# Kernel tuning notes

Measured on AMD Instinct MI355X. Metric: run time of the kernel, lower is better.

## Reference

```python
import jax, jax.numpy as jnp
import numpy as np

DIM = 1024
HEADS = 16
HEAD_DIM = DIM // HEADS
MLP_HIDDEN = int(DIM * 0.7)  # 716
EPS = 1e-5


def _ln(x, g, b):
    m = jnp.mean(x, axis=-1, keepdims=True)
    v = jnp.mean(jnp.square(x - m), axis=-1, keepdims=True)
    return (x - m) * jax.lax.rsqrt(v + EPS) * g + b


def setup_inputs() -> dict:
    key = jax.random.key(0)
    ks = jax.random.split(key, 8)
    B, N = 4, 1024
    x = jax.random.normal(ks[0], (B, N, DIM), dtype=jnp.float32)
    s = 0.02
    return {
        "x": x,
        "norm_g": jnp.ones((DIM,), jnp.float32),
        "norm_b": jnp.zeros((DIM,), jnp.float32),
        "W1": jax.random.normal(ks[1], (DIM, 3 * DIM + MLP_HIDDEN), jnp.float32) * s,
        "b1": jnp.zeros((3 * DIM + MLP_HIDDEN,), jnp.float32),
        "qn_g": jnp.ones((HEAD_DIM,), jnp.float32),
        "qn_b": jnp.zeros((HEAD_DIM,), jnp.float32),
        "kn_g": jnp.ones((HEAD_DIM,), jnp.float32),
        "kn_b": jnp.zeros((HEAD_DIM,), jnp.float32),
        "projW": jax.random.normal(ks[2], (DIM, DIM), jnp.float32) * s,
        "projb": jnp.zeros((DIM,), jnp.float32),
        "mlpW": jax.random.normal(ks[3], (MLP_HIDDEN, DIM), jnp.float32) * s,  # mlp_bias=False
        "W2": jax.random.normal(ks[4], (2 * DIM, DIM), jnp.float32) * s,
        "b2": jnp.zeros((DIM,), jnp.float32),
        "ls_g": jnp.full((DIM,), 1e-5, jnp.float32),
    }


def reference(x, norm_g, norm_b, W1, b1, qn_g, qn_b, kn_g, kn_b,
              projW, projb, mlpW, W2, b2, ls_g):
    B, N, C = x.shape
    norm_x = _ln(x, norm_g, norm_b)
    f1 = norm_x @ W1 + b1  # (B, N, 3*dim + mlp_hidden)
    qkv, mlp_hidden = f1[..., :3 * DIM], f1[..., 3 * DIM:]
    # (B, N, 3, H, hd) -> (3, B, H, N, hd)
    qkv = qkv.reshape(B, N, 3, HEADS, HEAD_DIM).transpose(2, 0, 3, 1, 4)
    q, k, v = qkv[0], qkv[1], qkv[2]
    q = _ln(q, qn_g, qn_b)
    k = _ln(k, kn_g, kn_b)
    attn = jnp.einsum('bhnd,bhmd->bhnm', q, k) * (HEAD_DIM ** -0.5)
    attn = jax.nn.softmax(attn, axis=-1)
    xo = jnp.einsum('bhnm,bhmd->bhnd', attn, v)
    xo = xo.transpose(0, 2, 1, 3).reshape(B, N, DIM)
    attn_out = xo @ projW + projb
    mlp_out = jax.nn.gelu(mlp_hidden, approximate=False) @ mlpW  # no bias
    combined = jnp.concatenate([attn_out, mlp_out], axis=-1)
    out = x + (combined @ W2 + b2) * ls_g
    return out
```

## Files before the change

### kernel.cpp

```cpp
#include <hip/hip_runtime.h>
#include <cstdint>
#include <cstddef>

typedef unsigned short u16;
typedef unsigned char u8;
typedef __attribute__((ext_vector_type(8))) u16 u16x8;
typedef __attribute__((ext_vector_type(8))) __bf16 bf16x8;
typedef __attribute__((ext_vector_type(4))) float f32x4;
typedef __attribute__((ext_vector_type(16))) float f32x16;
typedef __attribute__((ext_vector_type(4))) int i32x4;
typedef __attribute__((ext_vector_type(8))) int i32x8;

__device__ __forceinline__ u16 f2bf(float f) {
  unsigned u = __builtin_bit_cast(unsigned, f);
  return (u16)((u + 0x7FFFu + ((u >> 16) & 1u)) >> 16);
}
__device__ __forceinline__ float bf2f(u16 h) {
  return __builtin_bit_cast(float, (unsigned)h << 16);
}
__device__ __forceinline__ u8 f2fp8(float f) {
  return (u8)(__builtin_amdgcn_cvt_pk_fp8_f32(f, 0.f, 0, false) & 0xFF);
}
__device__ __forceinline__ f32x4 mfma16(u16x8 a, u16x8 b, f32x4 c) {
  return __builtin_amdgcn_mfma_f32_16x16x32_bf16(
      __builtin_bit_cast(bf16x8, a), __builtin_bit_cast(bf16x8, b), c, 0, 0, 0);
}
__device__ __forceinline__ void load_lds16(const void* g, void* l) {
  __builtin_amdgcn_global_load_lds(
      (const __attribute__((address_space(1))) void*)g,
      (__attribute__((address_space(3))) void*)l, 16, 0, 0);
}

__global__ __launch_bounds__(256) void k_trcvt_all(
    const float* __restrict__ W1, const float* __restrict__ projW,
    const float* __restrict__ mlpW, const float* __restrict__ W2,
    u8* __restrict__ W1t, u8* __restrict__ pWt, u8* __restrict__ mWt,
    u8* __restrict__ W2t) {
  __shared__ float t[32][33];
  const int L = blockIdx.x;
  const float* src;
  u8* dst;
  int R, C, dR, dC, bx, by;
  if (L < 3840) {
    src = W1; dst = W1t; R = 1024; C = 3788; dR = 1024; dC = 3840;
    bx = L % 120; by = L / 120;
  } else if (L < 4864) {
    int tq = L - 3840;
    src = projW; dst = pWt; R = 1024; C = 1024; dR = 1024; dC = 1024;
    bx = tq & 31; by = tq >> 5;
  } else if (L < 5632) {
    int tq = L - 4864;
    src = mlpW; dst = mWt; R = 716; C = 1024; dR = 768; dC = 1024;
    bx = tq & 31; by = tq >> 5;
  } else {
    int tq = L - 5632;
    src = W2; dst = W2t; R = 2048; C = 1024; dR = 2048; dC = 1024;
    bx = tq & 31; by = tq >> 5;
  }
  const int n0 = bx * 32, k0 = by * 32;
  const int tx = threadIdx.x & 31, ty = threadIdx.x >> 5;
#pragma unroll
  for (int j = 0; j < 4; ++j) {
    int kk = k0 + ty + 8 * j, nn = n0 + tx;
    float v = (kk < R && nn < C) ? src[(size_t)kk * C + nn] : 0.f;
    t[ty + 8 * j][tx] = v;
  }
  __syncthreads();
#pragma unroll
  for (int j = 0; j < 4; ++j) {
    int nn = n0 + ty + 8 * j, kk = k0 + tx;
    if (nn < dC && kk < dR) dst[(size_t)nn * dR + kk] = f2fp8(t[tx][ty + 8 * j]);
  }
}

__global__ __launch_bounds__(256) void k_trvt(const u16* __restrict__ f1,
                                              u16* __restrict__ vtb) {
  __shared__ u16 t[32][33];
  const int z = blockIdx.z;
  const int b = z >> 4, h = z & 15;
  const int d0 = blockIdx.x * 32, n0 = blockIdx.y * 32;
  const int tx = threadIdx.x & 31, ty = threadIdx.x >> 5;
#pragma unroll
  for (int j = 0; j < 4; ++j)
    t[ty + 8 * j][tx] =
        f1[(size_t)(b * 1024 + n0 + ty + 8 * j) * 3840 + 2048 + h * 64 + d0 + tx];
  __syncthreads();
#pragma unroll
  for (int j = 0; j < 4; ++j)
    vtb[(size_t)z * 65536 + (size_t)(d0 + ty + 8 * j) * 1024 + n0 + tx] =
        t[tx][ty + 8 * j];
}

__global__ __launch_bounds__(256) void k_lnx(const float* __restrict__ x,
                                             const float* __restrict__ g,
                                             const float* __restrict__ b,
                                             u8* __restrict__ out) {
  const int row = blockIdx.x, tid = threadIdx.x;
  float4 v = ((const float4*)(x + (size_t)row * 1024))[tid];
  float s = v.x + v.y + v.z + v.w;
  float ss = v.x * v.x + v.y * v.y + v.z * v.z + v.w * v.w;
#pragma unroll
  for (int off = 1; off < 64; off <<= 1) {
    s += __shfl_xor(s, off);
    ss += __shfl_xor(ss, off);
  }
  __shared__ float red[8];
  const int wid = tid >> 6, lane = tid & 63;
  if (lane == 0) { red[wid] = s; red[4 + wid] = ss; }
  __syncthreads();
  s = red[0] + red[1] + red[2] + red[3];
  ss = red[4] + red[5] + red[6] + red[7];
  const float mean = s * (1.f / 1024.f);
  const float var = ss * (1.f / 1024.f) - mean * mean;
  const float rstd = rsqrtf(var + 1e-5f);
  float4 gv = ((const float4*)g)[tid];
  float4 bv = ((const float4*)b)[tid];
  float y0 = (v.x - mean) * rstd * gv.x + bv.x;
  float y1 = (v.y - mean) * rstd * gv.y + bv.y;
  float y2 = (v.z - mean) * rstd * gv.z + bv.z;
  float y3 = (v.w - mean) * rstd * gv.w + bv.w;
  int pk = __builtin_amdgcn_cvt_pk_fp8_f32(y0, y1, 0, false);
  pk = __builtin_amdgcn_cvt_pk_fp8_f32(y2, y3, pk, true);
  ((int*)(out + (size_t)row * 1024))[tid] = pk;
}

__device__ __forceinline__ void gemm_fp8_core(const u8* __restrict__ A,
                                              const u8* __restrict__ B, int K,
                                              u8* Alds, u8* Blds,
                                              f32x16 (&acc)[2][2], int tid) {
  const int lane = tid & 63, wave = tid >> 6;
  const int h = lane >> 5, r32 = lane & 31;
  const int wrow = (wave >> 1) * 64, wcol = (wave & 1) * 64;
  const int srow0 = tid >> 2, spos = tid & 3;
  const int nk = K >> 6;
  for (int kt = 0; kt < nk; ++kt) {
#pragma unroll
    for (int p = 0; p < 2; ++p) {
      const int row = p * 64 + srow0;
      const int c = spos ^ ((row >> 1) & 3);
      const size_t go = (size_t)row * K + kt * 64 + c * 16;
      load_lds16(A + go, Alds + (p * 256 + tid) * 16);
      load_lds16(B + go, Blds + (p * 256 + tid) * 16);
    }
    __syncthreads();
    i32x8 af[2], bf[2];
#pragma unroll
    for (int t = 0; t < 2; ++t) {
      {
        const int row = wrow + t * 32 + r32;
        const int sw = (row >> 1) & 3;
        i32x4 lo = *(const i32x4*)(Alds + row * 64 + ((2 * h) ^ sw) * 16);
        i32x4 hi = *(const i32x4*)(Alds + row * 64 + ((2 * h + 1) ^ sw) * 16);
        i32x8 a;
        a[0] = lo[0]; a[1] = lo[1]; a[2] = lo[2]; a[3] = lo[3];
        a[4] = hi[0]; a[5] = hi[1]; a[6] = hi[2]; a[7] = hi[3];
        af[t] = a;
      }
      {
        const int row = wcol + t * 32 + r32;
        const int sw = (row >> 1) & 3;
        i32x4 lo = *(const i32x4*)(Blds + row * 64 + ((2 * h) ^ sw) * 16);
        i32x4 hi = *(const i32x4*)(Blds + row * 64 + ((2 * h + 1) ^ sw) * 16);
        i32x8 b8;
        b8[0] = lo[0]; b8[1] = lo[1]; b8[2] = lo[2]; b8[3] = lo[3];
        b8[4] = hi[0]; b8[5] = hi[1]; b8[6] = hi[2]; b8[7] = hi[3];
        bf[t] = b8;
      }
    }
#pragma unroll
    for (int i = 0; i < 2; ++i)
#pragma unroll
      for (int j = 0; j < 2; ++j)
        acc[i][j] = __builtin_amdgcn_mfma_scale_f32_32x32x64_f8f6f4(
            af[i], bf[j], acc[i][j], 0, 0, 0, 0x7F7F7F7F, 0, 0x7F7F7F7F);
    __syncthreads();
  }
}

__global__ __launch_bounds__(256) void k_gemm1(const u8* __restrict__ nx8,
                                               const u8* __restrict__ W1t,
                                               u16* __restrict__ f1,
                                               const float* __restrict__ b1) {
  __shared__ __align__(16) u8 Alds[128 * 64];
  __shared__ __align__(16) u8 Blds[128 * 64];
  const int tid = threadIdx.x, bm = blockIdx.y, bn = blockIdx.x;
  f32x16 acc[2][2];
#pragma unroll
  for (int i = 0; i < 2; ++i)
#pragma unroll
    for (int j = 0; j < 2; ++j)
#pragma unroll
      for (int r = 0; r < 16; ++r) acc[i][j][r] = 0.f;
  gemm_fp8_core(nx8 + (size_t)bm * 128 * 1024, W1t + (size_t)bn * 128 * 1024, 1024,
                Alds, Blds, acc, tid);
  const int lane = tid & 63, wave = tid >> 6;
  const int h = lane >> 5, r32 = lane & 31;
  const int wrow = (wave >> 1) * 64, wcol = (wave & 1) * 64;
#pragma unroll
  for (int i = 0; i < 2; ++i)
#pragma unroll
    for (int j = 0; j < 2; ++j) {
      const int col = bn * 128 + wcol + j * 32 + r32;
      const float bs = (col < 3788) ? b1[col] : 0.f;
#pragma unroll
      for (int r = 0; r < 16; ++r) {
        const int row = bm * 128 + wrow + i * 32 + 4 * h + (r & 3) + 8 * (r >> 2);
        f1[(size_t)row * 3840 + col] = f2bf(acc[i][j][r] + bs);
      }
    }
}

__global__ __launch_bounds__(256) void k_gemm_pm(
    const u8* __restrict__ xo, const u8* __restrict__ pWt,
    const u8* __restrict__ gel, const u8* __restrict__ mWt,
    u8* __restrict__ comb, const float* __restrict__ projb) {
  __shared__ __align__(16) u8 Alds[128 * 64];
  __shared__ __align__(16) u8 Blds[128 * 64];
  const int tid = threadIdx.x, bm = blockIdx.y, bnq = blockIdx.x;
  const u8* A;
  const u8* B;
  int K, colbase;
  const float* bias;
  if (bnq < 8) {
    A = xo + (size_t)bm * 128 * 1024;
    B = pWt + (size_t)bnq * 128 * 1024;
    K = 1024; colbase = bnq * 128; bias = projb;
  } else {
    A = gel + (size_t)bm * 128 * 768;
    B = mWt + (size_t)(bnq - 8) * 128 * 768;
    K = 768; colbase = 1024 + (bnq - 8) * 128; bias = nullptr;
  }
  f32x16 acc[2][2];
#pragma unroll
  for (int i = 0; i < 2; ++i)
#pragma unroll
    for (int j = 0; j < 2; ++j)
#pragma unroll
      for (int r = 0; r < 16; ++r) acc[i][j][r] = 0.f;
  gemm_fp8_core(A, B, K, Alds, Blds, acc, tid);
  const int lane = tid & 63, wave = tid >> 6;
  const int h = lane >> 5, r32 = lane & 31;
  const int wrow = (wave >> 1) * 64, wcol = (wave & 1) * 64;
#pragma unroll
  for (int i = 0; i < 2; ++i)
#pragma unroll
    for (int j = 0; j < 2; ++j) {
      const int col = colbase + wcol + j * 32 + r32;
      const float bs = (bias != nullptr) ? bias[col - colbase + colbase -
                                               (bias == projb ? 0 : 0)] : 0.f;
      const float bsv = (bias != nullptr) ? bias[wcol + j * 32 + r32 + 0 +
                                                 (colbase - colbase)] : 0.f;
      (void)bs;
#pragma unroll
      for (int r = 0; r < 16; ++r) {
        const int row = bm * 128 + wrow + i * 32 + 4 * h + (r & 3) + 8 * (r >> 2);
        float v = acc[i][j][r] + ((bias != nullptr) ? bias[col] : 0.f);
        (void)bsv;
        comb[(size_t)row * 2048 + col] = f2fp8(v);
      }
    }
}

__global__ __launch_bounds__(256) void k_gemm_fin(const u8* __restrict__ comb,
                                                  const u8* __restrict__ W2t,
                                                  float* __restrict__ out,
                                                  const float* __restrict__ b2,
                                                  const float* __restrict__ x,
                                                  const float* __restrict__ lsg) {
  __shared__ __align__(16) u8 Alds[128 * 64];
  __shared__ __align__(16) u8 Blds[128 * 64];
  const int tid = threadIdx.x, bm = blockIdx.y, bn = blockIdx.x;
  f32x16 acc[2][2];
#pragma unroll
  for (int i = 0; i < 2; ++i)
#pragma unroll
    for (int j = 0; j < 2; ++j)
#pragma unroll
      for (int r = 0; r < 16; ++r) acc[i][j][r] = 0.f;
  gemm_fp8_core(comb + (size_t)bm * 128 * 2048, W2t + (size_t)bn * 128 * 2048, 2048,
                Alds, Blds, acc, tid);
  const int lane = tid & 63, wave = tid >> 6;
  const int h = lane >> 5, r32 = lane & 31;
  const int wrow = (wave >> 1) * 64, wcol = (wave & 1) * 64;
#pragma unroll
  for (int i = 0; i < 2; ++i)
#pragma unroll
    for (int j = 0; j < 2; ++j) {
      const int col = bn * 128 + wcol + j * 32 + r32;
      const float bs = b2[col], ls = lsg[col];
#pragma unroll
      for (int r = 0; r < 16; ++r) {
        const int row = bm * 128 + wrow + i * 32 + 4 * h + (r & 3) + 8 * (r >> 2);
        out[(size_t)row * 1024 + col] =
            x[(size_t)row * 1024 + col] + (acc[i][j][r] + bs) * ls;
      }
    }
}

__global__ __launch_bounds__(256) void k_qkvgelu(const u16* __restrict__ f1,
                                                 const float* __restrict__ qg,
                                                 const float* __restrict__ qbb,
                                                 const float* __restrict__ kg,
                                                 const float* __restrict__ kbb,
                                                 u16* __restrict__ q,
                                                 u16* __restrict__ k,
                                                 u8* __restrict__ gel) {
  const int tid = threadIdx.x;
  if (blockIdx.x < 4096) {
    const int row = blockIdx.x;
    const int rem = tid >> 3;
    const int which = rem >> 4, h = rem & 15;
    const int e8 = (tid & 7) * 8;
    u16x8 xv = *(const u16x8*)(f1 + (size_t)row * 3840 + which * 1024 + h * 64 + e8);
    float xf[8];
    float s1 = 0.f, s2 = 0.f;
#pragma unroll
    for (int e = 0; e < 8; ++e) {
      xf[e] = bf2f(xv[e]);
      s1 += xf[e];
      s2 += xf[e] * xf[e];
    }
#pragma unroll
    for (int off = 1; off < 8; off <<= 1) {
      s1 += __shfl_xor(s1, off);
      s2 += __shfl_xor(s2, off);
    }
    const float mean = s1 * (1.f / 64.f);
    const float var = s2 * (1.f / 64.f) - mean * mean;
    const float rstd = rsqrtf(var + 1e-5f);
    const float* g = (which == 0) ? qg : kg;
    const float* bb = (which == 0) ? qbb : kbb;
    float4 g0 = ((const float4*)g)[e8 >> 2], g1 = ((const float4*)g)[(e8 >> 2) + 1];
    float4 b0 = ((const float4*)bb)[e8 >> 2], b1 = ((const float4*)bb)[(e8 >> 2) + 1];
    float gv[8] = {g0.x, g0.y, g0.z, g0.w, g1.x, g1.y, g1.z, g1.w};
    float bv[8] = {b0.x, b0.y, b0.z, b0.w, b1.x, b1.y, b1.z, b1.w};
    u16x8 o;
#pragma unroll
    for (int e = 0; e < 8; ++e) o[e] = f2bf((xf[e] - mean) * rstd * gv[e] + bv[e]);
    const int b = row >> 10, n = row & 1023;
    u16* dst = (which == 0) ? q : k;
    *(u16x8*)(dst + ((size_t)(b * 16 + h) * 1024 + n) * 64 + e8) = o;
  } else {
    const int id = (blockIdx.x - 4096) * 256 + tid;
    const int row = id / 96, c8 = id - row * 96;
    u16x8 xv = *(const u16x8*)(f1 + (size_t)row * 3840 + 3072 + c8 * 8);
    float rr[8];
#pragma unroll
    for (int e = 0; e < 8; ++e) {
      const int col = c8 * 8 + e;
      rr[e] = 0.f;
      if (col < 716) {
        float xx = bf2f(xv[e]);
        rr[e] = 0.5f * xx * (1.f + erff(xx * 0.70710678118654752f));
      }
    }
    int p0 = __builtin_amdgcn_cvt_pk_fp8_f32(rr[0], rr[1], 0, false);
    p0 = __builtin_amdgcn_cvt_pk_fp8_f32(rr[2], rr[3], p0, true);
    int p1 = __builtin_amdgcn_cvt_pk_fp8_f32(rr[4], rr[5], 0, false);
    p1 = __builtin_amdgcn_cvt_pk_fp8_f32(rr[6], rr[7], p1, true);
    uint2 pk;
    pk.x = (unsigned)p0;
    pk.y = (unsigned)p1;
    *(uint2*)(gel + (size_t)row * 768 + c8 * 8) = pk;
  }
}

__global__ __launch_bounds__(256) void k_flash(const u16* __restrict__ q,
                                               const u16* __restrict__ k,
                                               const u16* __restrict__ vt,
                                               u8* __restrict__ xo) {
  __shared__ __align__(16) u16 Kl[64 * 72];
  __shared__ __align__(16) u16 Vl[64 * 72];
  __shared__ __align__(16) u16 Pl[4 * 16 * 72];
  const int tid = threadIdx.x, wave = tid >> 6, lane = tid & 63;
  const int l15 = lane & 15, quad = lane >> 4;
  const int L = blockIdx.x;
  const int xcd = L & 7, idx = L >> 3;
  const int bh = xcd * 8 + (idx & 7), qt = idx >> 3;
  const int qrow0 = qt * 64 + wave * 16;
  const u16* qb = q + ((size_t)bh * 1024 + qrow0) * 64;
  const u16* kb = k + (size_t)bh * 1024 * 64;
  const u16* vb = vt + (size_t)bh * 64 * 1024;
  u16* Pw = Pl + wave * 16 * 72;

  u16x8 qf[2];
#pragma unroll
  for (int kk = 0; kk < 2; ++kk)
    qf[kk] = *(const u16x8*)(qb + (size_t)l15 * 64 + kk * 32 + quad * 8);

  f32x4 O[4];
  float lacc[4] = {0.f, 0.f, 0.f, 0.f};
#pragma unroll
  for (int dt = 0; dt < 4; ++dt) O[dt] = f32x4{0.f, 0.f, 0.f, 0.f};

  for (int kv = 0; kv < 16; ++kv) {
#pragma unroll
    for (int p = 0; p < 2; ++p) {
      const int ci = p * 256 + tid;
      const int r = ci >> 3, off = (ci & 7) * 8;
      *(u16x8*)(Kl + r * 72 + off) =
          *(const u16x8*)(kb + (size_t)(kv * 64 + r) * 64 + off);
      *(u16x8*)(Vl + r * 72 + off) =
          *(const u16x8*)(vb + (size_t)r * 1024 + kv * 64 + off);
    }
    __syncthreads();
    f32x4 S[4];
#pragma unroll
    for (int j = 0; j < 4; ++j) S[j] = f32x4{0.f, 0.f, 0.f, 0.f};
#pragma unroll
    for (int j = 0; j < 4; ++j)
#pragma unroll
      for (int kk = 0; kk < 2; ++kk) {
        u16x8 bfr = *(const u16x8*)(Kl + (16 * j + l15) * 72 + kk * 32 + quad * 8);
        S[j] = mfma16(qf[kk], bfr, S[j]);
      }
#pragma unroll
    for (int j = 0; j < 4; ++j)
#pragma unroll
      for (int r = 0; r < 4; ++r) {
        float pv = __expf(S[j][r] * 0.125f);
        lacc[r] += pv;
        Pw[(quad * 4 + r) * 72 + 16 * j + l15] = f2bf(pv);
      }
    __syncthreads();
#pragma unroll
    for (int c = 0; c < 2; ++c) {
      u16x8 pa = *(const u16x8*)(Pw + l15 * 72 + c * 32 + quad * 8);
#pragma unroll
      for (int dt = 0; dt < 4; ++dt) {
        u16x8 vf = *(const u16x8*)(Vl + (16 * dt + l15) * 72 + c * 32 + quad * 8);
        O[dt] = mfma16(pa, vf, O[dt]);
      }
    }
    __syncthreads();
  }
#pragma unroll
  for (int r = 0; r < 4; ++r) {
#pragma unroll
    for (int off = 1; off < 16; off <<= 1) lacc[r] += __shfl_xor(lacc[r], off);
  }
  const int b = bh >> 4, h = bh & 15;
#pragma unroll
  for (int r = 0; r < 4; ++r) {
    const float inv = 1.f / lacc[r];
    u8* orow = xo + (size_t)(b * 1024 + qrow0 + quad * 4 + r) * 1024 + h * 64;
#pragma unroll
    for (int dt = 0; dt < 4; ++dt) orow[16 * dt + l15] = f2fp8(O[dt][r] * inv);
  }
}

extern "C" void kernel_launch(void* const* d_in, const int* in_sizes, int n_in,
                              void* d_out, int out_size, void* d_ws, size_t ws_size,
                              hipStream_t stream) {
  (void)in_sizes; (void)n_in; (void)out_size; (void)ws_size;
  const float* x      = (const float*)d_in[0];
  const float* norm_g = (const float*)d_in[1];
  const float* norm_b = (const float*)d_in[2];
  const float* W1     = (const float*)d_in[3];
  const float* b1     = (const float*)d_in[4];
  const float* qn_g   = (const float*)d_in[5];
  const float* qn_b   = (const float*)d_in[6];
  const float* kn_g   = (const float*)d_in[7];
  const float* kn_b   = (const float*)d_in[8];
  const float* projW  = (const float*)d_in[9];
  const float* projb  = (const float*)d_in[10];
  const float* mlpW   = (const float*)d_in[11];
  const float* W2     = (const float*)d_in[12];
  const float* b2     = (const float*)d_in[13];
  const float* ls_g   = (const float*)d_in[14];

  char* ws = (char*)d_ws;
  u8*  W1t8 = (u8*)(ws + 0);
  u8*  pWt8 = (u8*)(ws + 3932160);
  u8*  mWt8 = (u8*)(ws + 4980736);
  u8*  W2t8 = (u8*)(ws + 5767168);
  u8*  nx8  = (u8*)(ws + 7864320);
  u16* f1   = (u16*)(ws + 12058624);
  u16* qbuf = (u16*)(ws + 43515904);
  u16* kbuf = (u16*)(ws + 51904512);
  u16* vtb  = (u16*)(ws + 60293120);
  u8*  gel8 = (u8*)(ws + 68681728);

  k_trcvt_all<<<7680, 256, 0, stream>>>(W1, projW, mlpW, W2, W1t8, pWt8, mWt8, W2t8);
  k_lnx<<<4096, 256, 0, stream>>>(x, norm_g, norm_b, nx8);
  k_gemm1<<<dim3(30, 32), 256, 0, stream>>>(nx8, W1t8, f1, b1);
  k_qkvgelu<<<5632, 256, 0, stream>>>(f1, qn_g, qn_b, kn_g, kn_b, qbuf, kbuf, gel8);
  k_trvt<<<dim3(2, 32, 64), 256, 0, stream>>>(f1, vtb);
  k_flash<<<1024, 256, 0, stream>>>(qbuf, kbuf, vtb, nx8);
  k_gemm_pm<<<dim3(16, 32), 256, 0, stream>>>(nx8, pWt8, gel8, mWt8, (u8*)f1, projb);
  k_gemm_fin<<<dim3(8, 32), 256, 0, stream>>>((u8*)f1, W2t8, (float*)d_out, b2, x,
                                              ls_g);
}
```

Measured before the change: 248.6 us.

## Halve GEMM and flash-attention tile heights, swizzle flash LDS with direct-to-LDS loads

The projection/MLP GEMM and the final GEMM now use 64-row M tiles through a new 64x128 FP8 core, which doubles their grid sizes to fill more CUs. Flash attention drops to 128-thread blocks covering 32 query rows, so twice as many blocks launch. Its K/V tiles are loaded straight into LDS through load_lds16 with an XOR swizzle in place of padded rows. The barrier before the PV stage becomes a per-wave LDS waitcnt. Each block now gets less reuse of B and K/V, and the waitcnt relies on the P buffer being private to each wave.

```diff
diff --git a/kernel.cpp b/kernel.cpp
--- a/kernel.cpp
+++ b/kernel.cpp
@@ -177,6 +177,56 @@
   }
 }
 
+__device__ __forceinline__ void gemm_fp8_core64(const u8* __restrict__ A,
+                                                const u8* __restrict__ B, int K,
+                                                u8* Alds, u8* Blds,
+                                                f32x16 (&acc)[2], int tid) {
+  const int lane = tid & 63, wave = tid >> 6;
+  const int h = lane >> 5, r32 = lane & 31;
+  const int wrow = (wave >> 1) * 32, wcol = (wave & 1) * 64;
+  const int nk = K >> 6;
+  for (int kt = 0; kt < nk; ++kt) {
+    {
+      const int r = tid >> 2, pos = tid & 3;
+      const int c = pos ^ ((r >> 1) & 3);
+      load_lds16(A + (size_t)r * K + kt * 64 + c * 16, Alds + tid * 16);
+    }
+#pragma unroll
+    for (int p = 0; p < 2; ++p) {
+      const int s = tid + 256 * p;
+      const int r = s >> 2, pos = s & 3;
+      const int c = pos ^ ((r >> 1) & 3);
+      load_lds16(B + (size_t)r * K + kt * 64 + c * 16, Blds + s * 16);
+    }
+    __syncthreads();
+    i32x8 af, bf[2];
+    {
+      const int row = wrow + r32;
+      const int sw = (row >> 1) & 3;
+      i32x4 lo = *(const i32x4*)(Alds + row * 64 + ((2 * h) ^ sw) * 16);
+      i32x4 hi = *(const i32x4*)(Alds + row * 64 + ((2 * h + 1) ^ sw) * 16);
+      af[0] = lo[0]; af[1] = lo[1]; af[2] = lo[2]; af[3] = lo[3];
+      af[4] = hi[0]; af[5] = hi[1]; af[6] = hi[2]; af[7] = hi[3];
+    }
+#pragma unroll
+    for (int t = 0; t < 2; ++t) {
+      const int row = wcol + t * 32 + r32;
+      const int sw = (row >> 1) & 3;
+      i32x4 lo = *(const i32x4*)(Blds + row * 64 + ((2 * h) ^ sw) * 16);
+      i32x4 hi = *(const i32x4*)(Blds + row * 64 + ((2 * h + 1) ^ sw) * 16);
+      i32x8 b8;
+      b8[0] = lo[0]; b8[1] = lo[1]; b8[2] = lo[2]; b8[3] = lo[3];
+      b8[4] = hi[0]; b8[5] = hi[1]; b8[6] = hi[2]; b8[7] = hi[3];
+      bf[t] = b8;
+    }
+#pragma unroll
+    for (int j = 0; j < 2; ++j)
+      acc[j] = __builtin_amdgcn_mfma_scale_f32_32x32x64_f8f6f4(
+          af, bf[j], acc[j], 0, 0, 0, 0x7F7F7F7F, 0, 0x7F7F7F7F);
+    __syncthreads();
+  }
+}
+
 __global__ __launch_bounds__(256) void k_gemm1(const u8* __restrict__ nx8,
                                                const u8* __restrict__ W1t,
                                                u16* __restrict__ f1,
@@ -214,7 +264,7 @@
     const u8* __restrict__ xo, const u8* __restrict__ pWt,
     const u8* __restrict__ gel, const u8* __restrict__ mWt,
     u8* __restrict__ comb, const float* __restrict__ projb) {
-  __shared__ __align__(16) u8 Alds[128 * 64];
+  __shared__ __align__(16) u8 Alds[64 * 64];
   __shared__ __align__(16) u8 Blds[128 * 64];
   const int tid = threadIdx.x, bm = blockIdx.y, bnq = blockIdx.x;
   const u8* A;
@@ -222,43 +272,36 @@
   int K, colbase;
   const float* bias;
   if (bnq < 8) {
-    A = xo + (size_t)bm * 128 * 1024;
+    A = xo + (size_t)bm * 64 * 1024;
     B = pWt + (size_t)bnq * 128 * 1024;
     K = 1024; colbase = bnq * 128; bias = projb;
   } else {
-    A = gel + (size_t)bm * 128 * 768;
+    A = gel + (size_t)bm * 64 * 768;
     B = mWt + (size_t)(bnq - 8) * 128 * 768;
     K = 768; colbase = 1024 + (bnq - 8) * 128; bias = nullptr;
   }
-  f32x16 acc[2][2];
-#pragma unroll
-  for (int i = 0; i < 2; ++i)
-#pragma unroll
-    for (int j = 0; j < 2; ++j)
-#pragma unroll
-      for (int r = 0; r < 16; ++r) acc[i][j][r] = 0.f;
-  gemm_fp8_core(A, B, K, Alds, Blds, acc, tid);
+  f32x16 acc[2];
+#pragma unroll
+  for (int j = 0; j < 2; ++j)
+#pragma unroll
+    for (int r = 0; r < 16; ++r) acc[j][r] = 0.f;
+  gemm_fp8_core64(A, B, K, Alds, Blds, acc, tid);
   const int lane = tid & 63, wave = tid >> 6;
   const int h = lane >> 5, r32 = lane & 31;
-  const int wrow = (wave >> 1) * 64, wcol = (wave & 1) * 64;
-#pragma unroll
-  for (int i = 0; i < 2; ++i)
-#pragma unroll
-    for (int j = 0; j < 2; ++j) {
-      const int col = colbase + wcol + j * 32 + r32;
-      const float bs = (bias != nullptr) ? bias[col - colbase + colbase -
-                                               (bias == projb ? 0 : 0)] : 0.f;
-      const float bsv = (bias != nullptr) ? bias[wcol + j * 32 + r32 + 0 +
-                                                 (colbase - colbase)] : 0.f;
-      (void)bs;
-#pragma unroll
-      for (int r = 0; r < 16; ++r) {
-        const int row = bm * 128 + wrow + i * 32 + 4 * h + (r & 3) + 8 * (r >> 2);
-        float v = acc[i][j][r] + ((bias != nullptr) ? bias[col] : 0.f);
-        (void)bsv;
-        comb[(size_t)row * 2048 + col] = f2fp8(v);
-      }
-    }
+  const int wrow = (wave >> 1) * 32, wcol = (wave & 1) * 64;
+#pragma unroll
+  for (int j = 0; j < 2; ++j) {
+    const int col = colbase + wcol + j * 32 + r32;
+    const float bs = (bias != nullptr) ? bias[col - colbase + colbase - colbase +
+                                              (bnq < 8 ? bnq * 128 : 0) - 
+                                              (bnq < 8 ? bnq * 128 : 0) + 
+                                              (wcol + j * 32 + r32)] : 0.f;
+#pragma unroll
+    for (int r = 0; r < 16; ++r) {
+      const int row = bm * 64 + wrow + 4 * h + (r & 3) + 8 * (r >> 2);
+      comb[(size_t)row * 2048 + col] = f2fp8(acc[j][r] + bs);
+    }
+  }
 }
 
 __global__ __launch_bounds__(256) void k_gemm_fin(const u8* __restrict__ comb,
@@ -267,34 +310,30 @@
                                                   const float* __restrict__ b2,
                                                   const float* __restrict__ x,
                                                   const float* __restrict__ lsg) {
-  __shared__ __align__(16) u8 Alds[128 * 64];
+  __shared__ __align__(16) u8 Alds[64 * 64];
   __shared__ __align__(16) u8 Blds[128 * 64];
   const int tid = threadIdx.x, bm = blockIdx.y, bn = blockIdx.x;
-  f32x16 acc[2][2];
-#pragma unroll
-  for (int i = 0; i < 2; ++i)
-#pragma unroll
-    for (int j = 0; j < 2; ++j)
-#pragma unroll
-      for (int r = 0; r < 16; ++r) acc[i][j][r] = 0.f;
-  gemm_fp8_core(comb + (size_t)bm * 128 * 2048, W2t + (size_t)bn * 128 * 2048, 2048,
-                Alds, Blds, acc, tid);
+  f32x16 acc[2];
+#pragma unroll
+  for (int j = 0; j < 2; ++j)
+#pragma unroll
+    for (int r = 0; r < 16; ++r) acc[j][r] = 0.f;
+  gemm_fp8_core64(comb + (size_t)bm * 64 * 2048, W2t + (size_t)bn * 128 * 2048, 2048,
+                  Alds, Blds, acc, tid);
   const int lane = tid & 63, wave = tid >> 6;
   const int h = lane >> 5, r32 = lane & 31;
-  const int wrow = (wave >> 1) * 64, wcol = (wave & 1) * 64;
-#pragma unroll
-  for (int i = 0; i < 2; ++i)
-#pragma unroll
-    for (int j = 0; j < 2; ++j) {
-      const int col = bn * 128 + wcol + j * 32 + r32;
-      const float bs = b2[col], ls = lsg[col];
-#pragma unroll
-      for (int r = 0; r < 16; ++r) {
-        const int row = bm * 128 + wrow + i * 32 + 4 * h + (r & 3) + 8 * (r >> 2);
-        out[(size_t)row * 1024 + col] =
-            x[(size_t)row * 1024 + col] + (acc[i][j][r] + bs) * ls;
-      }
-    }
+  const int wrow = (wave >> 1) * 32, wcol = (wave & 1) * 64;
+#pragma unroll
+  for (int j = 0; j < 2; ++j) {
+    const int col = bn * 128 + wcol + j * 32 + r32;
+    const float bs = b2[col], ls = lsg[col];
+#pragma unroll
+    for (int r = 0; r < 16; ++r) {
+      const int row = bm * 64 + wrow + 4 * h + (r & 3) + 8 * (r >> 2);
+      out[(size_t)row * 1024 + col] =
+          x[(size_t)row * 1024 + col] + (acc[j][r] + bs) * ls;
+    }
+  }
 }
 
 __global__ __launch_bounds__(256) void k_qkvgelu(const u16* __restrict__ f1,
@@ -365,43 +404,43 @@
   }
 }
 
-__global__ __launch_bounds__(256) void k_flash(const u16* __restrict__ q,
+__global__ __launch_bounds__(128) void k_flash(const u16* __restrict__ q,
                                                const u16* __restrict__ k,
                                                const u16* __restrict__ vt,
                                                u8* __restrict__ xo) {
-  __shared__ __align__(16) u16 Kl[64 * 72];
-  __shared__ __align__(16) u16 Vl[64 * 72];
-  __shared__ __align__(16) u16 Pl[4 * 16 * 72];
+  __shared__ __align__(16) u16 Kl[64 * 64];
+  __shared__ __align__(16) u16 Vl[64 * 64];
+  __shared__ __align__(16) u16 Pl[2 * 16 * 64];
   const int tid = threadIdx.x, wave = tid >> 6, lane = tid & 63;
   const int l15 = lane & 15, quad = lane >> 4;
   const int L = blockIdx.x;
-  const int xcd = L & 7, idx = L >> 3;
-  const int bh = xcd * 8 + (idx & 7), qt = idx >> 3;
-  const int qrow0 = qt * 64 + wave * 16;
+  const int xcd = L & 7, i = L >> 3;
+  const int bh = xcd * 8 + (i & 7), qt = i >> 3;
+  const int qrow0 = qt * 32 + wave * 16;
   const u16* qb = q + ((size_t)bh * 1024 + qrow0) * 64;
   const u16* kb = k + (size_t)bh * 1024 * 64;
   const u16* vb = vt + (size_t)bh * 64 * 1024;
-  u16* Pw = Pl + wave * 16 * 72;
+  u16* Pw = Pl + wave * 16 * 64;
 
   u16x8 qf[2];
 #pragma unroll
   for (int kk = 0; kk < 2; ++kk)
-    qf[kk] = *(const u16x8*)(qb + (size_t)l15 * 64 + kk * 32 + quad * 8);
+    qf[kk] = *(const u16x8*)(qb + (size_t)l15 * 64 + (kk * 4 + quad) * 8);
 
   f32x4 O[4];
   float lacc[4] = {0.f, 0.f, 0.f, 0.f};
 #pragma unroll
   for (int dt = 0; dt < 4; ++dt) O[dt] = f32x4{0.f, 0.f, 0.f, 0.f};
 
+  const int pl7 = l15 & 7;
   for (int kv = 0; kv < 16; ++kv) {
 #pragma unroll
-    for (int p = 0; p < 2; ++p) {
-      const int ci = p * 256 + tid;
-      const int r = ci >> 3, off = (ci & 7) * 8;
-      *(u16x8*)(Kl + r * 72 + off) =
-          *(const u16x8*)(kb + (size_t)(kv * 64 + r) * 64 + off);
-      *(u16x8*)(Vl + r * 72 + off) =
-          *(const u16x8*)(vb + (size_t)r * 1024 + kv * 64 + off);
+    for (int p = 0; p < 4; ++p) {
+      const int s = tid + 128 * p;
+      const int r = s >> 3, pos = s & 7;
+      const int c = pos ^ (r & 7);
+      load_lds16(kb + (size_t)(kv * 64 + r) * 64 + c * 8, Kl + s * 8);
+      load_lds16(vb + (size_t)r * 1024 + kv * 64 + c * 8, Vl + s * 8);
     }
     __syncthreads();
     f32x4 S[4];
@@ -411,7 +450,8 @@
     for (int j = 0; j < 4; ++j)
 #pragma unroll
       for (int kk = 0; kk < 2; ++kk) {
-        u16x8 bfr = *(const u16x8*)(Kl + (16 * j + l15) * 72 + kk * 32 + quad * 8);
+        const int pos = (kk * 4 + quad) ^ pl7;
+        u16x8 bfr = *(const u16x8*)(Kl + (16 * j + l15) * 64 + pos * 8);
         S[j] = mfma16(qf[kk], bfr, S[j]);
       }
 #pragma unroll
@@ -420,15 +460,18 @@
       for (int r = 0; r < 4; ++r) {
         float pv = __expf(S[j][r] * 0.125f);
         lacc[r] += pv;
-        Pw[(quad * 4 + r) * 72 + 16 * j + l15] = f2bf(pv);
-      }
-    __syncthreads();
+        const int prow = quad * 4 + r;
+        const int pc = 2 * j + (l15 >> 3);
+        Pw[prow * 64 + (pc ^ (prow & 7)) * 8 + pl7] = f2bf(pv);
+      }
+    __builtin_amdgcn_s_waitcnt(0xC07F);
 #pragma unroll
     for (int c = 0; c < 2; ++c) {
-      u16x8 pa = *(const u16x8*)(Pw + l15 * 72 + c * 32 + quad * 8);
+      const int pos = (c * 4 + quad) ^ pl7;
+      u16x8 pa = *(const u16x8*)(Pw + l15 * 64 + pos * 8);
 #pragma unroll
       for (int dt = 0; dt < 4; ++dt) {
-        u16x8 vf = *(const u16x8*)(Vl + (16 * dt + l15) * 72 + c * 32 + quad * 8);
+        u16x8 vf = *(const u16x8*)(Vl + (16 * dt + l15) * 64 + pos * 8);
         O[dt] = mfma16(pa, vf, O[dt]);
       }
     }
@@ -486,8 +529,8 @@
   k_gemm1<<<dim3(30, 32), 256, 0, stream>>>(nx8, W1t8, f1, b1);
   k_qkvgelu<<<5632, 256, 0, stream>>>(f1, qn_g, qn_b, kn_g, kn_b, qbuf, kbuf, gel8);
   k_trvt<<<dim3(2, 32, 64), 256, 0, stream>>>(f1, vtb);
-  k_flash<<<1024, 256, 0, stream>>>(qbuf, kbuf, vtb, nx8);
-  k_gemm_pm<<<dim3(16, 32), 256, 0, stream>>>(nx8, pWt8, gel8, mWt8, (u8*)f1, projb);
-  k_gemm_fin<<<dim3(8, 32), 256, 0, stream>>>((u8*)f1, W2t8, (float*)d_out, b2, x,
+  k_flash<<<2048, 128, 0, stream>>>(qbuf, kbuf, vtb, nx8);
+  k_gemm_pm<<<dim3(16, 64), 256, 0, stream>>>(nx8, pWt8, gel8, mWt8, (u8*)f1, projb);
+  k_gemm_fin<<<dim3(8, 64), 256, 0, stream>>>((u8*)f1, W2t8, (float*)d_out, b2, x,
                                               ls_g);
 }
```

New measurement: 238.1 us. 4.2% less time.
